# Kernel optimization log

Hardware: AMD Instinct MI355X
Metric: run time of the kernel (lower is better)

The kernel has to match this reference:

```python
import jax, jax.numpy as jnp
import numpy as np

EPS = 1e-5

def _ln(x, g, b):
    m = x.mean(-1, keepdims=True)
    v = ((x - m) ** 2).mean(-1, keepdims=True)
    return (x - m) * jax.lax.rsqrt(v + EPS) * g + b

def _glu(z):
    a, g = jnp.split(z, 2, axis=-1)
    return a * jax.nn.sigmoid(g)

def setup_inputs() -> dict:
    key = jax.random.key(0)
    ks = jax.random.split(key, 8)
    B, T, V, I, H = 64, 512, 32, 64, 64
    s = 0.02
    return {
        "x": jax.random.normal(ks[0], (B, T, V, I), dtype=jnp.float32),
        # weight GRN: (V*I) -> V
        "wg_W1": jax.random.normal(ks[1], (V * I, V), dtype=jnp.float32) * s,
        "wg_b1": jnp.zeros((V,), jnp.float32),
        "wg_W2": jax.random.normal(ks[2], (V, V), dtype=jnp.float32) * s,
        "wg_b2": jnp.zeros((V,), jnp.float32),
        "wg_Wg": jax.random.normal(ks[3], (V, 2 * V), dtype=jnp.float32) * s,
        "wg_bg": jnp.zeros((2 * V,), jnp.float32),
        "wg_Ws": jax.random.normal(ks[4], (V * I, V), dtype=jnp.float32) * s,
        "wg_bs": jnp.zeros((V,), jnp.float32),
        "wg_gamma": jnp.ones((V,), jnp.float32),
        "wg_beta": jnp.zeros((V,), jnp.float32),
        # per-variable GRNs, batched over V: I -> H (I == H, skip is identity)
        "v_W1": jax.random.normal(ks[5], (V, I, H), dtype=jnp.float32) * s,
        "v_b1": jnp.zeros((V, H), jnp.float32),
        "v_W2": jax.random.normal(ks[6], (V, H, H), dtype=jnp.float32) * s,
        "v_b2": jnp.zeros((V, H), jnp.float32),
        "v_Wg": jax.random.normal(ks[7], (V, H, 2 * H), dtype=jnp.float32) * s,
        "v_bg": jnp.zeros((V, 2 * H), jnp.float32),
        "v_gamma": jnp.ones((V, H), jnp.float32),
        "v_beta": jnp.zeros((V, H), jnp.float32),
    }

def reference(x, wg_W1, wg_b1, wg_W2, wg_b2, wg_Wg, wg_bg, wg_Ws, wg_bs,
              wg_gamma, wg_beta, v_W1, v_b1, v_W2, v_b2, v_Wg, v_bg,
              v_gamma, v_beta):
    B, T, V, I = x.shape
    # ---- variable-selection weights GRN on flattened input ----
    flat = x.reshape(B, T, V * I)                       # [B,T,V*I]
    skip = flat @ wg_Ws + wg_bs                          # [B,T,V] (proj skip: sizes differ)
    h = jax.nn.elu(flat @ wg_W1 + wg_b1)
    h = h @ wg_W2 + wg_b2
    w = _ln(skip + _glu(h @ wg_Wg + wg_bg), wg_gamma, wg_beta)
    w = jax.nn.softmax(w, axis=-1)                       # [B,T,V]
    # ---- per-variable GRNs, batched over V (skip = x since I == H) ----
    h = jax.nn.elu(jnp.einsum('btvi,vih->btvh', x, v_W1) + v_b1)
    h = jnp.einsum('btvh,vhk->btvk', h, v_W2) + v_b2
    g = jnp.einsum('btvh,vhk->btvk', h, v_Wg) + v_bg     # [B,T,V,2H]
    pv = _ln(x + _glu(g), v_gamma, v_beta)               # [B,T,V,H]
    # ---- softmax-weighted combination over variables ----
    return jnp.einsum('btv,btvh->bth', w, pv)            # [B,T,H]
```

## Files before the change

kernel.cpp:

```cpp
#include <hip/hip_runtime.h>

#define NT   32768
#define NV   32
#define DI   64
#define VI   2048

typedef __attribute__((ext_vector_type(8)))  short short8;
typedef __attribute__((ext_vector_type(16))) float floatx16;

#define MFMA32(a,b,c) __builtin_amdgcn_mfma_f32_32x32x16_bf16(a, b, c, 0, 0, 0)

#define WS_S      0
#define WS_WBUF   8388608
#define WS_WCOMBT 12582912
#define WS_WAV    12845056
#define WS_WC2    13926400
#define WS_BC2    13934592

static __device__ __forceinline__ unsigned short f2bf(float f) {
    union { float f; unsigned u; } v; v.f = f;
    unsigned r = v.u + 0x7FFFu + ((v.u >> 16) & 1u);
    return (unsigned short)(r >> 16);
}
static __device__ __forceinline__ unsigned pk2bf(float lo, float hi) {
    return (unsigned)f2bf(lo) | ((unsigned)f2bf(hi) << 16);
}
static __device__ __forceinline__ float elu1(float v) {
    return (v > 0.f) ? v : (__expf(v) - 1.f);
}
static __device__ __forceinline__ float bflo(unsigned v) {
    union { unsigned u; float f; } t; t.u = v << 16; return t.f;
}
static __device__ __forceinline__ float bfhi(unsigned v) {
    union { unsigned u; float f; } t; t.u = v & 0xFFFF0000u; return t.f;
}

__global__ void k0_prep(const float* __restrict__ wg_W1, const float* __restrict__ wg_Ws,
                        const float* __restrict__ wg_W2, const float* __restrict__ wg_b2,
                        const float* __restrict__ wg_Wg, const float* __restrict__ wg_bg,
                        const float* __restrict__ v_W1, const float* __restrict__ v_b1,
                        const float* __restrict__ v_W2, const float* __restrict__ v_b2,
                        const float* __restrict__ v_Wg, const float* __restrict__ v_bg,
                        unsigned short* __restrict__ WcombT, unsigned short* __restrict__ wAv,
                        float* __restrict__ Wc2, float* __restrict__ bc2) {
    int tid = blockIdx.x * blockDim.x + threadIdx.x;
    int np  = gridDim.x * blockDim.x;
    for (int i = tid; i < 64 * 2048; i += np) {
        int n = i >> 11, k = i & 2047;
        float val = (n < 32) ? wg_Ws[k * 32 + n] : wg_W1[k * 32 + (n - 32)];
        WcombT[i] = f2bf(val);
    }
    for (int i = tid; i < 32 * 64 * 88; i += np) {
        int v  = i / (64 * 88);
        int rm = i - v * (64 * 88);
        int h  = rm / 88, c = rm - h * 88;
        float val = 0.f;
        if (c < 64)       val = v_W1[(v * 64 + c) * 64 + h];
        else if (c == 64) val = v_b1[v * 64 + h];
        wAv[v * 16896 + h * 88 + c] = f2bf(val);
    }
    for (int i = tid; i < 32 * 128 * 88; i += np) {
        int v  = i / (128 * 88);
        int rm = i - v * (128 * 88);
        int n  = rm / 88, c = rm - n * 88;
        float acc = 0.f;
        if (c < 64) {
            #pragma unroll 8
            for (int k = 0; k < 64; ++k)
                acc += v_W2[(v * 64 + c) * 64 + k] * v_Wg[(v * 64 + k) * 128 + n];
        } else if (c == 64) {
            #pragma unroll 8
            for (int k = 0; k < 64; ++k)
                acc += v_b2[v * 64 + k] * v_Wg[(v * 64 + k) * 128 + n];
            acc += v_bg[v * 128 + n];
        }
        wAv[v * 16896 + (64 + n) * 88 + c] = f2bf(acc);
    }
    for (int i = tid; i < 32 * 64 + 64; i += np) {
        if (i < 2048) {
            int j = i >> 6, n = i & 63;
            float acc = 0.f;
            #pragma unroll 8
            for (int k = 0; k < 32; ++k) acc += wg_W2[j * 32 + k] * wg_Wg[k * 64 + n];
            Wc2[i] = acc;
        } else {
            int n = i - 2048;
            float acc = 0.f;
            #pragma unroll 8
            for (int k = 0; k < 32; ++k) acc += wg_b2[k] * wg_Wg[k * 64 + n];
            bc2[n] = acc + wg_bg[n];
        }
    }
}

__launch_bounds__(256, 4)
__global__ void k1_wgemm(const float* __restrict__ x, const unsigned short* __restrict__ WcombT,
                         const float* __restrict__ wg_bs, const float* __restrict__ wg_b1,
                         float* __restrict__ S) {
    __shared__ float Cbuf[4 * 64 * 33];
    int tid  = threadIdx.x;
    int wv   = tid >> 6;
    int lane = tid & 63;
    int l31  = lane & 31, s = lane >> 5;
    int tile = blockIdx.x;
    long tok = (long)tile * 32 + l31;

    const float*          xrow = x + tok * VI + wv * 512 + s * 8;
    const unsigned short* a0p  = WcombT + (l31)      * 2048 + wv * 512 + s * 8;
    const unsigned short* a1p  = WcombT + (l31 + 32) * 2048 + wv * 512 + s * 8;

    floatx16 acc0 = {}; floatx16 acc1 = {};
    #pragma unroll 4
    for (int ks = 0; ks < 32; ++ks) {
        int ko = ks * 16;
        short8 af0 = *(const short8*)(a0p + ko);
        short8 af1 = *(const short8*)(a1p + ko);
        float4 xa = *(const float4*)(xrow + ko);
        float4 xb = *(const float4*)(xrow + ko + 4);
        union { unsigned u[4]; short8 s8; } bp;
        bp.u[0] = pk2bf(xa.x, xa.y);
        bp.u[1] = pk2bf(xa.z, xa.w);
        bp.u[2] = pk2bf(xb.x, xb.y);
        bp.u[3] = pk2bf(xb.z, xb.w);
        acc0 = MFMA32(af0, bp.s8, acc0);
        acc1 = MFMA32(af1, bp.s8, acc1);
    }
    float* cb = Cbuf + wv * (64 * 33);
    #pragma unroll
    for (int reg = 0; reg < 16; ++reg) {
        int r0 = (reg & 3) + 8 * (reg >> 2) + 4 * s;
        cb[(r0)*33 + l31]      = acc0[reg];
        cb[(r0 + 32)*33 + l31] = acc1[reg];
    }
    __syncthreads();
    int n  = tid & 63;
    int tb = (tid >> 6) * 8;
    #pragma unroll
    for (int g = 0; g < 8; ++g) {
        int t = tb + g;
        float v = Cbuf[0*2112 + n*33 + t] + Cbuf[1*2112 + n*33 + t]
                + Cbuf[2*2112 + n*33 + t] + Cbuf[3*2112 + n*33 + t];
        if (n < 32) v += wg_bs[n];
        else        v = elu1(v + wg_b1[n - 32]);
        S[((long)tile * 32 + t) * 64 + n] = v;
    }
}

__launch_bounds__(256, 4)
__global__ void k2_token(const float* __restrict__ S,
                         const float* __restrict__ Wc2, const float* __restrict__ bc2,
                         const float* __restrict__ wg_gamma, const float* __restrict__ wg_beta,
                         float* __restrict__ wout) {
    int tid = threadIdx.x;
    int wv = tid >> 6, lane = tid & 63;
    int l31 = lane & 31;
    long t = (long)blockIdx.x * 4 + wv;
    float sv = S[t * 64 + lane];
    float z = bc2[lane];
    #pragma unroll
    for (int k = 0; k < 32; ++k) {
        float hk = __shfl(sv, 32 + k);
        z += hk * Wc2[k * 64 + lane];
    }
    float za   = __shfl(z, l31);
    float zg   = __shfl(z, l31 + 32);
    float skip = __shfl(sv, l31);
    float y = skip + za / (1.f + __expf(-zg));
    float s1 = y;
    #pragma unroll
    for (int m = 1; m <= 16; m <<= 1) s1 += __shfl_xor(s1, m);
    float mean = s1 * (1.f / 32.f);
    float d = y - mean;
    float s2 = d * d;
    #pragma unroll
    for (int m = 1; m <= 16; m <<= 1) s2 += __shfl_xor(s2, m);
    float rinv  = rsqrtf(s2 * (1.f / 32.f) + 1e-5f);
    float logit = d * rinv * wg_gamma[l31] + wg_beta[l31];
    float mx = logit;
    #pragma unroll
    for (int m = 1; m <= 16; m <<= 1) mx = fmaxf(mx, __shfl_xor(mx, m));
    float e = __expf(logit - mx);
    float se = e;
    #pragma unroll
    for (int m = 1; m <= 16; m <<= 1) se += __shfl_xor(se, m);
    if (lane < 32) wout[t * 32 + lane] = e / se;
}

static __device__ __forceinline__ void tile_to_bfrags(const float* t16, int sh,
                                                      short8* f0, short8* f1) {
    unsigned P[8];
    #pragma unroll
    for (int i = 0; i < 8; ++i) P[i] = pk2bf(t16[2 * i], t16[2 * i + 1]);
    unsigned X[8];
    #pragma unroll
    for (int i = 0; i < 8; ++i) X[i] = (unsigned)__shfl_xor((int)P[i], 32);
    union { unsigned u[4]; short8 s8; } a, b;
    a.u[0] = sh ? X[2] : P[0];  a.u[1] = sh ? X[3] : P[1];
    a.u[2] = sh ? P[2] : X[0];  a.u[3] = sh ? P[3] : X[1];
    b.u[0] = sh ? X[6] : P[4];  b.u[1] = sh ? X[7] : P[5];
    b.u[2] = sh ? P[6] : X[4];  b.u[3] = sh ? P[7] : X[5];
    *f0 = a.s8; *f1 = b.s8;
}

__launch_bounds__(256, 3)
__global__ void k3_vgrn(const float* __restrict__ x, const unsigned short* __restrict__ wAv,
                        const float* __restrict__ v_gamma, const float* __restrict__ v_beta,
                        const float* __restrict__ wbuf, float* __restrict__ out) {
    __shared__ __align__(16) unsigned short wA[192 * 88];
    __shared__ __align__(16) unsigned short xt[128 * 72];
    __shared__ float gb[128];
    int tid  = threadIdx.x;
    int wv   = tid >> 6, lane = tid & 63;
    int l31  = lane & 31, s = lane >> 5;
    int vg   = blockIdx.x & 3;
    int tb   = blockIdx.x >> 2;
    int tl   = wv * 32 + l31;
    long tokg = (long)tb * 128 + tl;

    float outacc[32];
    #pragma unroll
    for (int i = 0; i < 32; ++i) outacc[i] = 0.f;

    union { unsigned u[4]; short8 s8; } onef;
    onef.u[0] = (s == 0) ? 0x00003F80u : 0u;
    onef.u[1] = 0; onef.u[2] = 0; onef.u[3] = 0;

    const unsigned short* wArow = wA + l31 * 88 + s * 8;
    int srow = tid >> 1, shalf = tid & 1;

    for (int j8 = 0; j8 < 8; ++j8) {
        int v = vg * 8 + j8;
        __syncthreads();
        {
            const uint4* src = (const uint4*)(wAv + (long)v * 16896);
            uint4* dst = (uint4*)wA;
            for (int c = tid; c < 2112; c += 256) dst[c] = src[c];
        }
        {
            const float* xs = x + ((long)tb * 128 + srow) * VI + v * 64 + shalf * 32;
            unsigned short* xd = xt + srow * 72 + shalf * 32;
            #pragma unroll
            for (int q = 0; q < 4; ++q) {
                float4 a = ((const float4*)xs)[2 * q];
                float4 b = ((const float4*)xs)[2 * q + 1];
                uint4 w;
                w.x = pk2bf(a.x, a.y); w.y = pk2bf(a.z, a.w);
                w.z = pk2bf(b.x, b.y); w.w = pk2bf(b.z, b.w);
                ((uint4*)xd)[q] = w;
            }
        }
        if (tid < 128) {
            int h = tid >> 1;
            gb[tid] = (tid & 1) ? v_beta[v * 64 + h] : v_gamma[v * 64 + h];
        }
        __syncthreads();

        union { short8 s8; unsigned u[4]; } xb[4];
        #pragma unroll
        for (int ks = 0; ks < 4; ++ks)
            xb[ks].s8 = *(const short8*)(xt + tl * 72 + ks * 16 + s * 8);

        floatx16 h1a0 = {}, h1a1 = {};
        #pragma unroll
        for (int ks = 0; ks < 5; ++ks) {
            short8 b = (ks < 4) ? xb[ks].s8 : onef.s8;
            h1a0 = MFMA32(*(const short8*)(wArow + 0    + ks * 16), b, h1a0);
            h1a1 = MFMA32(*(const short8*)(wArow + 2816 + ks * 16), b, h1a1);
        }
        short8 h1b[4];
        {
            float t16[16];
            #pragma unroll
            for (int r = 0; r < 16; ++r) t16[r] = elu1(h1a0[r]);
            tile_to_bfrags(t16, s, &h1b[0], &h1b[1]);
            #pragma unroll
            for (int r = 0; r < 16; ++r) t16[r] = elu1(h1a1[r]);
            tile_to_bfrags(t16, s, &h1b[2], &h1b[3]);
        }
        floatx16 g0 = {}, g1 = {}, g2 = {}, g3 = {};
        #pragma unroll
        for (int ks = 0; ks < 5; ++ks) {
            short8 b = (ks < 4) ? h1b[ks] : onef.s8;
            g0 = MFMA32(*(const short8*)(wArow + 2 * 2816 + ks * 16), b, g0);
            g1 = MFMA32(*(const short8*)(wArow + 3 * 2816 + ks * 16), b, g1);
            g2 = MFMA32(*(const short8*)(wArow + 4 * 2816 + ks * 16), b, g2);
            g3 = MFMA32(*(const short8*)(wArow + 5 * 2816 + ks * 16), b, g3);
        }
        unsigned ownu[4][2], Xu[4][2];
        #pragma unroll
        for (int kk = 0; kk < 4; ++kk) {
            #pragma unroll
            for (int d = 0; d < 2; ++d) {
                ownu[kk][d] = s ? xb[kk].u[2 + d] : xb[kk].u[d];
                unsigned R  = s ? xb[kk].u[d]     : xb[kk].u[2 + d];
                Xu[kk][d]   = (unsigned)__shfl_xor((int)R, 32);
            }
        }
        float y[32];
        #pragma unroll
        for (int r = 0; r < 16; ++r) {
            int a = r >> 2, b_ = r & 3, d = b_ >> 1, kk = a >> 1;
            bool odd = (a & 1);
            unsigned v0 = odd ? (s ? ownu[kk][d]     : Xu[kk][d])
                              : (s ? Xu[kk][d]       : ownu[kk][d]);
            unsigned v1 = odd ? (s ? ownu[2+kk][d]   : Xu[2+kk][d])
                              : (s ? Xu[2+kk][d]     : ownu[2+kk][d]);
            float sk0 = (b_ & 1) ? bfhi(v0) : bflo(v0);
            float sk1 = (b_ & 1) ? bfhi(v1) : bflo(v1);
            y[r]      = sk0 + g0[r] / (1.f + __expf(-g2[r]));
            y[16 + r] = sk1 + g1[r] / (1.f + __expf(-g3[r]));
        }
        float s1 = 0.f;
        #pragma unroll
        for (int i = 0; i < 32; ++i) s1 += y[i];
        s1 += __shfl_xor(s1, 32);
        float mean = s1 * (1.f / 64.f);
        float s2 = 0.f;
        #pragma unroll
        for (int i = 0; i < 32; ++i) { float d = y[i] - mean; s2 += d * d; }
        s2 += __shfl_xor(s2, 32);
        float rinv = rsqrtf(s2 * (1.f / 64.f) + 1e-5f);
        float wvv = wbuf[tokg * 32 + v];
        #pragma unroll
        for (int r = 0; r < 16; ++r) {
            int hr = (r & 3) + 8 * (r >> 2) + 4 * s;
            float pv0 = (y[r]      - mean) * rinv * gb[2*hr]      + gb[2*hr + 1];
            float pv1 = (y[16 + r] - mean) * rinv * gb[2*(hr+32)] + gb[2*(hr+32) + 1];
            outacc[r]      += wvv * pv0;
            outacc[16 + r] += wvv * pv1;
        }
    }
    #pragma unroll
    for (int r = 0; r < 16; ++r) {
        int hr = (r & 3) + 8 * (r >> 2) + 4 * s;
        atomicAdd(out + tokg * 64 + hr,      outacc[r]);
        atomicAdd(out + tokg * 64 + 32 + hr, outacc[16 + r]);
    }
}

extern "C" void kernel_launch(void* const* d_in, const int* in_sizes, int n_in,
                              void* d_out, int out_size, void* d_ws, size_t ws_size,
                              hipStream_t stream) {
    const float* x        = (const float*)d_in[0];
    const float* wg_W1    = (const float*)d_in[1];
    const float* wg_b1    = (const float*)d_in[2];
    const float* wg_W2    = (const float*)d_in[3];
    const float* wg_b2    = (const float*)d_in[4];
    const float* wg_Wg    = (const float*)d_in[5];
    const float* wg_bg    = (const float*)d_in[6];
    const float* wg_Ws    = (const float*)d_in[7];
    const float* wg_bs    = (const float*)d_in[8];
    const float* wg_gamma = (const float*)d_in[9];
    const float* wg_beta  = (const float*)d_in[10];
    const float* v_W1     = (const float*)d_in[11];
    const float* v_b1     = (const float*)d_in[12];
    const float* v_W2     = (const float*)d_in[13];
    const float* v_b2     = (const float*)d_in[14];
    const float* v_Wg     = (const float*)d_in[15];
    const float* v_bg     = (const float*)d_in[16];
    const float* v_gamma  = (const float*)d_in[17];
    const float* v_beta   = (const float*)d_in[18];
    (void)in_sizes; (void)n_in; (void)ws_size;

    char* ws = (char*)d_ws;
    float* S               = (float*)(ws + WS_S);
    float* wbuf            = (float*)(ws + WS_WBUF);
    unsigned short* WcombT = (unsigned short*)(ws + WS_WCOMBT);
    unsigned short* wAv    = (unsigned short*)(ws + WS_WAV);
    float* Wc2             = (float*)(ws + WS_WC2);
    float* bc2             = (float*)(ws + WS_BC2);
    float* out             = (float*)d_out;

    hipMemsetAsync(d_out, 0, (size_t)out_size * sizeof(float), stream);
    k0_prep<<<512, 256, 0, stream>>>(wg_W1, wg_Ws, wg_W2, wg_b2, wg_Wg, wg_bg,
                                     v_W1, v_b1, v_W2, v_b2, v_Wg, v_bg,
                                     WcombT, wAv, Wc2, bc2);
    k1_wgemm<<<1024, 256, 0, stream>>>(x, WcombT, wg_bs, wg_b1, S);
    k2_token<<<8192, 256, 0, stream>>>(S, Wc2, bc2, wg_gamma, wg_beta, wbuf);
    k3_vgrn<<<1024, 256, 0, stream>>>(x, wAv, v_gamma, v_beta, wbuf, out);
}
```

Measured before the change: 774.5 us.

## Double-buffer x tiles in LDS and pre-swizzle weights into MFMA fragment layout

k0 now writes the bf16 weights in a fragment-ordered layout, so k1 and k3 can load MFMA A operands straight from global memory with contiguous 16-byte loads. k1 moves from a per-wave K split with an LDS reduction to 64-token tiles, where x is converted to bf16 and double-buffered in LDS while register prefetch of the next chunk overlaps the MFMAs. k3 stops copying per-variable weights into LDS each iteration, double-buffers the x tile and gamma/beta, and loads the softmax weights once. The cost is lower occupancy in k1 (launch bounds 2), more LDS per block, and weight reads now depend on global cache hits.

New measurement: 917.2 us. 1.18x slower.

```diff
diff --git a/kernel.cpp b/kernel.cpp
--- a/kernel.cpp
+++ b/kernel.cpp
@@ -14,8 +14,8 @@
 #define WS_WBUF   8388608
 #define WS_WCOMBT 12582912
 #define WS_WAV    12845056
-#define WS_WC2    13926400
-#define WS_BC2    13934592
+#define WS_WC2    13828096
+#define WS_BC2    13836288
 
 static __device__ __forceinline__ unsigned short f2bf(float f) {
     union { float f; unsigned u; } v; v.f = f;
@@ -45,36 +45,43 @@
                         float* __restrict__ Wc2, float* __restrict__ bc2) {
     int tid = blockIdx.x * blockDim.x + threadIdx.x;
     int np  = gridDim.x * blockDim.x;
-    for (int i = tid; i < 64 * 2048; i += np) {
-        int n = i >> 11, k = i & 2047;
-        float val = (n < 32) ? wg_Ws[k * 32 + n] : wg_W1[k * 32 + (n - 32)];
-        WcombT[i] = f2bf(val);
-    }
-    for (int i = tid; i < 32 * 64 * 88; i += np) {
-        int v  = i / (64 * 88);
-        int rm = i - v * (64 * 88);
-        int h  = rm / 88, c = rm - h * 88;
+    for (int f = tid; f < 131072; f += np) {
+        int e = f & 7, l = (f >> 3) & 31, s = (f >> 8) & 1;
+        int ks = (f >> 9) & 15, m = (f >> 13) & 1, c8 = f >> 14;
+        int k = c8 * 256 + ks * 16 + s * 8 + e;
+        int mr = m * 32 + l;
+        float val = (mr < 32) ? wg_Ws[k * 32 + mr] : wg_W1[k * 32 + (mr - 32)];
+        WcombT[f] = f2bf(val);
+    }
+    for (int i = tid; i < 32 * 80 * 64; i += np) {
+        int mr = i & 63;
+        int rest = i >> 6;
+        int kk = rest % 80;
+        int v  = rest / 80;
         float val = 0.f;
-        if (c < 64)       val = v_W1[(v * 64 + c) * 64 + h];
-        else if (c == 64) val = v_b1[v * 64 + h];
-        wAv[v * 16896 + h * 88 + c] = f2bf(val);
-    }
-    for (int i = tid; i < 32 * 128 * 88; i += np) {
-        int v  = i / (128 * 88);
-        int rm = i - v * (128 * 88);
-        int n  = rm / 88, c = rm - n * 88;
+        if (kk < 64)       val = v_W1[(v * 64 + kk) * 64 + mr];
+        else if (kk == 64) val = v_b1[v * 64 + mr];
+        int t6 = mr >> 5, l = mr & 31, ks = kk >> 4, s = (kk >> 3) & 1, e = kk & 7;
+        wAv[v * 15360 + ((t6 * 5 + ks) * 2 + s) * 256 + l * 8 + e] = f2bf(val);
+    }
+    for (int i = tid; i < 32 * 80 * 128; i += np) {
+        int n = i & 127;
+        int rest = i >> 7;
+        int kk = rest % 80;
+        int v  = rest / 80;
         float acc = 0.f;
-        if (c < 64) {
+        if (kk < 64) {
             #pragma unroll 8
-            for (int k = 0; k < 64; ++k)
-                acc += v_W2[(v * 64 + c) * 64 + k] * v_Wg[(v * 64 + k) * 128 + n];
-        } else if (c == 64) {
+            for (int k2 = 0; k2 < 64; ++k2)
+                acc += v_W2[(v * 64 + kk) * 64 + k2] * v_Wg[(v * 64 + k2) * 128 + n];
+        } else if (kk == 64) {
             #pragma unroll 8
-            for (int k = 0; k < 64; ++k)
-                acc += v_b2[v * 64 + k] * v_Wg[(v * 64 + k) * 128 + n];
+            for (int k2 = 0; k2 < 64; ++k2)
+                acc += v_b2[v * 64 + k2] * v_Wg[(v * 64 + k2) * 128 + n];
             acc += v_bg[v * 128 + n];
         }
-        wAv[v * 16896 + (64 + n) * 88 + c] = f2bf(acc);
+        int t6 = 2 + (n >> 5), l = n & 31, ks = kk >> 4, s = (kk >> 3) & 1, e = kk & 7;
+        wAv[v * 15360 + ((t6 * 5 + ks) * 2 + s) * 256 + l * 8 + e] = f2bf(acc);
     }
     for (int i = tid; i < 32 * 64 + 64; i += np) {
         if (i < 2048) {
@@ -93,56 +100,81 @@
     }
 }
 
-__launch_bounds__(256, 4)
+#define K1_BUF 33792
+__launch_bounds__(256, 2)
 __global__ void k1_wgemm(const float* __restrict__ x, const unsigned short* __restrict__ WcombT,
                          const float* __restrict__ wg_bs, const float* __restrict__ wg_b1,
                          float* __restrict__ S) {
-    __shared__ float Cbuf[4 * 64 * 33];
+    __shared__ __align__(16) unsigned char lds[2 * K1_BUF];
     int tid  = threadIdx.x;
-    int wv   = tid >> 6;
-    int lane = tid & 63;
+    int wv   = tid >> 6, lane = tid & 63;
     int l31  = lane & 31, s = lane >> 5;
-    int tile = blockIdx.x;
-    long tok = (long)tile * 32 + l31;
-
-    const float*          xrow = x + tok * VI + wv * 512 + s * 8;
-    const unsigned short* a0p  = WcombT + (l31)      * 2048 + wv * 512 + s * 8;
-    const unsigned short* a1p  = WcombT + (l31 + 32) * 2048 + wv * 512 + s * 8;
-
-    floatx16 acc0 = {}; floatx16 acc1 = {};
-    #pragma unroll 4
-    for (int ks = 0; ks < 32; ++ks) {
-        int ko = ks * 16;
-        short8 af0 = *(const short8*)(a0p + ko);
-        short8 af1 = *(const short8*)(a1p + ko);
-        float4 xa = *(const float4*)(xrow + ko);
-        float4 xb = *(const float4*)(xrow + ko + 4);
-        union { unsigned u[4]; short8 s8; } bp;
-        bp.u[0] = pk2bf(xa.x, xa.y);
-        bp.u[1] = pk2bf(xa.z, xa.w);
-        bp.u[2] = pk2bf(xb.x, xb.y);
-        bp.u[3] = pk2bf(xb.z, xb.w);
-        acc0 = MFMA32(af0, bp.s8, acc0);
-        acc1 = MFMA32(af1, bp.s8, acc1);
-    }
-    float* cb = Cbuf + wv * (64 * 33);
+    int m    = wv & 1, th = wv >> 1;
+    long tok0 = (long)blockIdx.x * 64;
+
+    int r  = tid >> 2;
+    int c4 = tid & 3;
+    const float* xrow = x + (tok0 + r) * VI + c4 * 4;
+
+    float4 pf[16];
+    #pragma unroll
+    for (int j = 0; j < 16; ++j) pf[j] = *(const float4*)(xrow + j * 16);
+    {
+        unsigned char* dst = lds;
+        #pragma unroll
+        for (int j = 0; j < 16; ++j) {
+            int mm = c4 + 4 * j;
+            int ks = mm >> 2, ss = (mm >> 1) & 1, e4 = mm & 1;
+            int blk = ((r >> 5) * 16 + ks) * 2 + ss;
+            uint2 w; w.x = pk2bf(pf[j].x, pf[j].y); w.y = pk2bf(pf[j].z, pf[j].w);
+            *(uint2*)(dst + blk * 528 + (r & 31) * 16 + e4 * 8) = w;
+        }
+    }
+    __syncthreads();
+
+    floatx16 acc = {};
+    for (int c8 = 0; c8 < 8; ++c8) {
+        if (c8 < 7) {
+            const float* xp = xrow + (c8 + 1) * 256;
+            #pragma unroll
+            for (int j = 0; j < 16; ++j) pf[j] = *(const float4*)(xp + j * 16);
+        }
+        const unsigned char* bb = lds + (c8 & 1) * K1_BUF;
+        const unsigned short* ab = WcombT + (((long)(c8 * 2 + m) * 16) * 2) * 32 * 8;
+        #pragma unroll
+        for (int ks = 0; ks < 16; ++ks) {
+            short8 af = *(const short8*)(ab + ((ks * 2 + s) * 32 + l31) * 8);
+            short8 bf = *(const short8*)(bb + ((th * 16 + ks) * 2 + s) * 528 + l31 * 16);
+            acc = MFMA32(af, bf, acc);
+        }
+        if (c8 < 7) {
+            unsigned char* dst = lds + ((c8 + 1) & 1) * K1_BUF;
+            #pragma unroll
+            for (int j = 0; j < 16; ++j) {
+                int mm = c4 + 4 * j;
+                int ks = mm >> 2, ss = (mm >> 1) & 1, e4 = mm & 1;
+                int blk = ((r >> 5) * 16 + ks) * 2 + ss;
+                uint2 w; w.x = pk2bf(pf[j].x, pf[j].y); w.y = pk2bf(pf[j].z, pf[j].w);
+                *(uint2*)(dst + blk * 528 + (r & 31) * 16 + e4 * 8) = w;
+            }
+        }
+        __syncthreads();
+    }
+    float* Cbuf = (float*)lds;
     #pragma unroll
     for (int reg = 0; reg < 16; ++reg) {
         int r0 = (reg & 3) + 8 * (reg >> 2) + 4 * s;
-        cb[(r0)*33 + l31]      = acc0[reg];
-        cb[(r0 + 32)*33 + l31] = acc1[reg];
+        Cbuf[(m * 32 + r0) * 65 + th * 32 + l31] = acc[reg];
     }
     __syncthreads();
-    int n  = tid & 63;
-    int tb = (tid >> 6) * 8;
-    #pragma unroll
-    for (int g = 0; g < 8; ++g) {
-        int t = tb + g;
-        float v = Cbuf[0*2112 + n*33 + t] + Cbuf[1*2112 + n*33 + t]
-                + Cbuf[2*2112 + n*33 + t] + Cbuf[3*2112 + n*33 + t];
-        if (n < 32) v += wg_bs[n];
-        else        v = elu1(v + wg_b1[n - 32]);
-        S[((long)tile * 32 + t) * 64 + n] = v;
+    int mr = tid & 63, tg = tid >> 6;
+    float bias = (mr < 32) ? wg_bs[mr] : wg_b1[mr - 32];
+    #pragma unroll
+    for (int g = 0; g < 16; ++g) {
+        int t = tg * 16 + g;
+        float v = Cbuf[mr * 65 + t] + bias;
+        if (mr >= 32) v = elu1(v);
+        S[(tok0 + t) * 64 + mr] = v;
     }
 }
 
@@ -168,24 +200,25 @@
     float y = skip + za / (1.f + __expf(-zg));
     float s1 = y;
     #pragma unroll
-    for (int m = 1; m <= 16; m <<= 1) s1 += __shfl_xor(s1, m);
+    for (int mm = 1; mm <= 16; mm <<= 1) s1 += __shfl_xor(s1, mm);
     float mean = s1 * (1.f / 32.f);
     float d = y - mean;
     float s2 = d * d;
     #pragma unroll
-    for (int m = 1; m <= 16; m <<= 1) s2 += __shfl_xor(s2, m);
+    for (int mm = 1; mm <= 16; mm <<= 1) s2 += __shfl_xor(s2, mm);
     float rinv  = rsqrtf(s2 * (1.f / 32.f) + 1e-5f);
     float logit = d * rinv * wg_gamma[l31] + wg_beta[l31];
     float mx = logit;
     #pragma unroll
-    for (int m = 1; m <= 16; m <<= 1) mx = fmaxf(mx, __shfl_xor(mx, m));
+    for (int mm = 1; mm <= 16; mm <<= 1) mx = fmaxf(mx, __shfl_xor(mx, mm));
     float e = __expf(logit - mx);
     float se = e;
     #pragma unroll
-    for (int m = 1; m <= 16; m <<= 1) se += __shfl_xor(se, m);
+    for (int mm = 1; mm <= 16; mm <<= 1) se += __shfl_xor(se, mm);
     if (lane < 32) wout[t * 32 + lane] = e / se;
 }
 
+#define K3_BUF 16896
 static __device__ __forceinline__ void tile_to_bfrags(const float* t16, int sh,
                                                       short8* f0, short8* f1) {
     unsigned P[8];
@@ -206,9 +239,8 @@
 __global__ void k3_vgrn(const float* __restrict__ x, const unsigned short* __restrict__ wAv,
                         const float* __restrict__ v_gamma, const float* __restrict__ v_beta,
                         const float* __restrict__ wbuf, float* __restrict__ out) {
-    __shared__ __align__(16) unsigned short wA[192 * 88];
-    __shared__ __align__(16) unsigned short xt[128 * 72];
-    __shared__ float gb[128];
+    __shared__ __align__(16) unsigned char xls[2 * K3_BUF];
+    __shared__ float gb[2][128];
     int tid  = threadIdx.x;
     int wv   = tid >> 6, lane = tid & 63;
     int l31  = lane & 31, s = lane >> 5;
@@ -225,66 +257,75 @@
     onef.u[0] = (s == 0) ? 0x00003F80u : 0u;
     onef.u[1] = 0; onef.u[2] = 0; onef.u[3] = 0;
 
-    const unsigned short* wArow = wA + l31 * 88 + s * 8;
-    int srow = tid >> 1, shalf = tid & 1;
+    union { float4 q[2]; float f[8]; } wv8;
+    wv8.q[0] = *(const float4*)(wbuf + tokg * 32 + vg * 8);
+    wv8.q[1] = *(const float4*)(wbuf + tokg * 32 + vg * 8 + 4);
+
+    int r   = tid >> 1;
+    int hf  = tid & 1;
+    const float* xrbase = x + ((long)tb * 128 + r) * VI + vg * 8 * 64 + hf * 32;
+
+    float4 pf[8];
+    #pragma unroll
+    for (int q = 0; q < 8; ++q) pf[q] = *(const float4*)(xrbase + q * 4);
+    {
+        unsigned char* dst = xls;
+        #pragma unroll
+        for (int q = 0; q < 4; ++q) {
+            int ks = 2 * hf + (q >> 1), ss = q & 1;
+            int blk = ((r >> 5) * 4 + ks) * 2 + ss;
+            uint4 w;
+            w.x = pk2bf(pf[2*q].x,   pf[2*q].y);   w.y = pk2bf(pf[2*q].z,   pf[2*q].w);
+            w.z = pk2bf(pf[2*q+1].x, pf[2*q+1].y); w.w = pk2bf(pf[2*q+1].z, pf[2*q+1].w);
+            *(uint4*)(dst + blk * 528 + (r & 31) * 16) = w;
+        }
+    }
+    if (tid < 128) {
+        int h = tid >> 1;
+        gb[0][tid] = (tid & 1) ? v_beta[(vg * 8) * 64 + h] : v_gamma[(vg * 8) * 64 + h];
+    }
+    __syncthreads();
 
     for (int j8 = 0; j8 < 8; ++j8) {
         int v = vg * 8 + j8;
-        __syncthreads();
-        {
-            const uint4* src = (const uint4*)(wAv + (long)v * 16896);
-            uint4* dst = (uint4*)wA;
-            for (int c = tid; c < 2112; c += 256) dst[c] = src[c];
-        }
-        {
-            const float* xs = x + ((long)tb * 128 + srow) * VI + v * 64 + shalf * 32;
-            unsigned short* xd = xt + srow * 72 + shalf * 32;
-            #pragma unroll
-            for (int q = 0; q < 4; ++q) {
-                float4 a = ((const float4*)xs)[2 * q];
-                float4 b = ((const float4*)xs)[2 * q + 1];
-                uint4 w;
-                w.x = pk2bf(a.x, a.y); w.y = pk2bf(a.z, a.w);
-                w.z = pk2bf(b.x, b.y); w.w = pk2bf(b.z, b.w);
-                ((uint4*)xd)[q] = w;
-            }
-        }
-        if (tid < 128) {
-            int h = tid >> 1;
-            gb[tid] = (tid & 1) ? v_beta[v * 64 + h] : v_gamma[v * 64 + h];
-        }
-        __syncthreads();
-
+        const unsigned char* xb_base = xls + (j8 & 1) * K3_BUF;
         union { short8 s8; unsigned u[4]; } xb[4];
         #pragma unroll
         for (int ks = 0; ks < 4; ++ks)
-            xb[ks].s8 = *(const short8*)(xt + tl * 72 + ks * 16 + s * 8);
-
+            xb[ks].s8 = *(const short8*)(xb_base + ((wv * 4 + ks) * 2 + s) * 528 + l31 * 16);
+
+        if (j8 < 7) {
+            const float* xp = xrbase + (j8 + 1) * 64;
+            #pragma unroll
+            for (int q = 0; q < 8; ++q) pf[q] = *(const float4*)(xp + q * 4);
+        }
+
+        const unsigned short* wvb = wAv + (long)v * 15360;
         floatx16 h1a0 = {}, h1a1 = {};
         #pragma unroll
         for (int ks = 0; ks < 5; ++ks) {
             short8 b = (ks < 4) ? xb[ks].s8 : onef.s8;
-            h1a0 = MFMA32(*(const short8*)(wArow + 0    + ks * 16), b, h1a0);
-            h1a1 = MFMA32(*(const short8*)(wArow + 2816 + ks * 16), b, h1a1);
+            h1a0 = MFMA32(*(const short8*)(wvb + ((0 * 5 + ks) * 2 + s) * 256 + l31 * 8), b, h1a0);
+            h1a1 = MFMA32(*(const short8*)(wvb + ((1 * 5 + ks) * 2 + s) * 256 + l31 * 8), b, h1a1);
         }
         short8 h1b[4];
         {
             float t16[16];
             #pragma unroll
-            for (int r = 0; r < 16; ++r) t16[r] = elu1(h1a0[r]);
+            for (int rr = 0; rr < 16; ++rr) t16[rr] = elu1(h1a0[rr]);
             tile_to_bfrags(t16, s, &h1b[0], &h1b[1]);
             #pragma unroll
-            for (int r = 0; r < 16; ++r) t16[r] = elu1(h1a1[r]);
+            for (int rr = 0; rr < 16; ++rr) t16[rr] = elu1(h1a1[rr]);
             tile_to_bfrags(t16, s, &h1b[2], &h1b[3]);
         }
         floatx16 g0 = {}, g1 = {}, g2 = {}, g3 = {};
         #pragma unroll
         for (int ks = 0; ks < 5; ++ks) {
             short8 b = (ks < 4) ? h1b[ks] : onef.s8;
-            g0 = MFMA32(*(const short8*)(wArow + 2 * 2816 + ks * 16), b, g0);
-            g1 = MFMA32(*(const short8*)(wArow + 3 * 2816 + ks * 16), b, g1);
-            g2 = MFMA32(*(const short8*)(wArow + 4 * 2816 + ks * 16), b, g2);
-            g3 = MFMA32(*(const short8*)(wArow + 5 * 2816 + ks * 16), b, g3);
+            g0 = MFMA32(*(const short8*)(wvb + ((2 * 5 + ks) * 2 + s) * 256 + l31 * 8), b, g0);
+            g1 = MFMA32(*(const short8*)(wvb + ((3 * 5 + ks) * 2 + s) * 256 + l31 * 8), b, g1);
+            g2 = MFMA32(*(const short8*)(wvb + ((4 * 5 + ks) * 2 + s) * 256 + l31 * 8), b, g2);
+            g3 = MFMA32(*(const short8*)(wvb + ((5 * 5 + ks) * 2 + s) * 256 + l31 * 8), b, g3);
         }
         unsigned ownu[4][2], Xu[4][2];
         #pragma unroll
@@ -298,8 +339,8 @@
         }
         float y[32];
         #pragma unroll
-        for (int r = 0; r < 16; ++r) {
-            int a = r >> 2, b_ = r & 3, d = b_ >> 1, kk = a >> 1;
+        for (int rr = 0; rr < 16; ++rr) {
+            int a = rr >> 2, b_ = rr & 3, d = b_ >> 1, kk = a >> 1;
             bool odd = (a & 1);
             unsigned v0 = odd ? (s ? ownu[kk][d]     : Xu[kk][d])
                               : (s ? Xu[kk][d]       : ownu[kk][d]);
@@ -307,8 +348,8 @@
                               : (s ? Xu[2+kk][d]     : ownu[2+kk][d]);
             float sk0 = (b_ & 1) ? bfhi(v0) : bflo(v0);
             float sk1 = (b_ & 1) ? bfhi(v1) : bflo(v1);
-            y[r]      = sk0 + g0[r] / (1.f + __expf(-g2[r]));
-            y[16 + r] = sk1 + g1[r] / (1.f + __expf(-g3[r]));
+            y[rr]      = sk0 + g0[rr] / (1.f + __expf(-g2[rr]));
+            y[16 + rr] = sk1 + g1[rr] / (1.f + __expf(-g3[rr]));
         }
         float s1 = 0.f;
         #pragma unroll
@@ -320,21 +361,39 @@
         for (int i = 0; i < 32; ++i) { float d = y[i] - mean; s2 += d * d; }
         s2 += __shfl_xor(s2, 32);
         float rinv = rsqrtf(s2 * (1.f / 64.f) + 1e-5f);
-        float wvv = wbuf[tokg * 32 + v];
-        #pragma unroll
-        for (int r = 0; r < 16; ++r) {
-            int hr = (r & 3) + 8 * (r >> 2) + 4 * s;
-            float pv0 = (y[r]      - mean) * rinv * gb[2*hr]      + gb[2*hr + 1];
-            float pv1 = (y[16 + r] - mean) * rinv * gb[2*(hr+32)] + gb[2*(hr+32) + 1];
-            outacc[r]      += wvv * pv0;
-            outacc[16 + r] += wvv * pv1;
-        }
-    }
-    #pragma unroll
-    for (int r = 0; r < 16; ++r) {
-        int hr = (r & 3) + 8 * (r >> 2) + 4 * s;
-        atomicAdd(out + tokg * 64 + hr,      outacc[r]);
-        atomicAdd(out + tokg * 64 + 32 + hr, outacc[16 + r]);
+        float wvv = wv8.f[j8];
+        #pragma unroll
+        for (int rr = 0; rr < 16; ++rr) {
+            int hr = (rr & 3) + 8 * (rr >> 2) + 4 * s;
+            float pv0 = (y[rr]      - mean) * rinv * gb[j8 & 1][2*hr]        + gb[j8 & 1][2*hr + 1];
+            float pv1 = (y[16 + rr] - mean) * rinv * gb[j8 & 1][2*(hr+32)]   + gb[j8 & 1][2*(hr+32) + 1];
+            outacc[rr]      += wvv * pv0;
+            outacc[16 + rr] += wvv * pv1;
+        }
+        if (j8 < 7) {
+            unsigned char* dst = xls + ((j8 + 1) & 1) * K3_BUF;
+            #pragma unroll
+            for (int q = 0; q < 4; ++q) {
+                int ks = 2 * hf + (q >> 1), ss = q & 1;
+                int blk = ((r >> 5) * 4 + ks) * 2 + ss;
+                uint4 w;
+                w.x = pk2bf(pf[2*q].x,   pf[2*q].y);   w.y = pk2bf(pf[2*q].z,   pf[2*q].w);
+                w.z = pk2bf(pf[2*q+1].x, pf[2*q+1].y); w.w = pk2bf(pf[2*q+1].z, pf[2*q+1].w);
+                *(uint4*)(dst + blk * 528 + (r & 31) * 16) = w;
+            }
+            if (tid < 128) {
+                int h = tid >> 1;
+                gb[(j8 + 1) & 1][tid] = (tid & 1) ? v_beta[(v + 1) * 64 + h]
+                                                  : v_gamma[(v + 1) * 64 + h];
+            }
+            __syncthreads();
+        }
+    }
+    #pragma unroll
+    for (int rr = 0; rr < 16; ++rr) {
+        int hr = (rr & 3) + 8 * (rr >> 2) + 4 * s;
+        atomicAdd(out + tokg * 64 + hr,      outacc[rr]);
+        atomicAdd(out + tokg * 64 + 32 + hr, outacc[16 + rr]);
     }
 }
 
@@ -372,10 +431,10 @@
     float* out             = (float*)d_out;
 
     hipMemsetAsync(d_out, 0, (size_t)out_size * sizeof(float), stream);
-    k0_prep<<<512, 256, 0, stream>>>(wg_W1, wg_Ws, wg_W2, wg_b2, wg_Wg, wg_bg,
-                                     v_W1, v_b1, v_W2, v_b2, v_Wg, v_bg,
-                                     WcombT, wAv, Wc2, bc2);
-    k1_wgemm<<<1024, 256, 0, stream>>>(x, WcombT, wg_bs, wg_b1, S);
+    k0_prep<<<1024, 256, 0, stream>>>(wg_W1, wg_Ws, wg_W2, wg_b2, wg_Wg, wg_bg,
+                                      v_W1, v_b1, v_W2, v_b2, v_Wg, v_bg,
+                                      WcombT, wAv, Wc2, bc2);
+    k1_wgemm<<<512, 256, 0, stream>>>(x, WcombT, wg_bs, wg_b1, S);
     k2_token<<<8192, 256, 0, stream>>>(S, Wc2, bc2, wg_gamma, wg_beta, wbuf);
     k3_vgrn<<<1024, 256, 0, stream>>>(x, wAv, v_gamma, v_beta, wbuf, out);
 }
```
